# Performance work log

Hardware: AMD Instinct MI355X
Metric: run time of the kernel (lower is better)

The kernel has to match this reference:

```python
import jax, jax.numpy as jnp
import numpy as np

B, T, D = 2, 2048, 1024
HEADS, UNITS = 16, 64
OUT_DIM = 1024
_LARGE_BIAS = 10000.0


def _uniform(key, shape, fan_in, fan_out):
    limit = np.sqrt(6.0 / (fan_in + fan_out))
    return jax.random.uniform(key, shape, jnp.float32, -limit, limit)


def setup_inputs() -> dict:
    key = jax.random.key(0)
    kx, kq, kk, kv, ko = jax.random.split(key, 5)
    x = jax.random.normal(kx, (B, T, D), jnp.float32)
    mask = jnp.ones((B, T), jnp.int32)
    Wq = _uniform(kq, (D, HEADS * UNITS), D, UNITS)
    Wk = _uniform(kk, (D, HEADS * UNITS), D, UNITS)
    Wv = _uniform(kv, (D, HEADS * UNITS), D, UNITS)
    Wo = _uniform(ko, (HEADS * UNITS, OUT_DIM), HEADS * UNITS, OUT_DIM)
    return {"x": x, "mask": mask, "Wq": Wq, "Wk": Wk, "Wv": Wv, "Wo": Wo}


def reference(x, mask, Wq, Wk, Wv, Wo):
    m = mask.astype(x.dtype)                      # [B, T]
    x = x * m[:, :, None]                         # zero padded positions
    b, t, _ = x.shape
    # projections, split heads: [B, T, H, U]
    q = (x @ Wq).reshape(b, t, HEADS, UNITS)
    k = (x @ Wk).reshape(b, t, HEADS, UNITS)
    v = (x @ Wv).reshape(b, t, HEADS, UNITS)
    # logits[b,h,i,j] = sum_u q[b,i,h,u] k[b,j,h,u]
    logits = jnp.einsum('bihu,bjhu->bhij', q, k) / np.sqrt(UNITS).astype(x.dtype)
    # causal (forward) mask: subtract large bias above the diagonal
    causal = jnp.triu(jnp.full((t, t), _LARGE_BIAS, x.dtype), k=1)
    logits = logits - causal
    # padding mask on key axis
    logits = logits - ((1.0 - m) * _LARGE_BIAS)[:, None, None, :]
    weights = jax.nn.softmax(logits, axis=-1)     # [B, H, T, T]
    attended = jnp.einsum('bhij,bjhu->bihu', weights, v)
    attended = attended.reshape(b, t, HEADS * UNITS)
    return attended @ Wo                          # [B, T, OUT_DIM]
```

## Files before the change

kernel.cpp:

```cpp
#include <hip/hip_runtime.h>
#include <stdint.h>
#include <stddef.h>

#define B_ 2
#define T_ 2048
#define D_ 1024
#define H_ 16
#define U_ 64
#define M_ (B_ * T_)
#define N_ (H_ * U_)

typedef __attribute__((ext_vector_type(4))) float f32x4;
typedef __attribute__((ext_vector_type(8))) short s16x8;
typedef __attribute__((ext_vector_type(8))) __bf16 b16x8;

static_assert(sizeof(s16x8) == 16, "frag size");

__device__ __forceinline__ unsigned short f2bf(float f) {
  unsigned int u = __float_as_uint(f);
  u += 0x7FFFu + ((u >> 16) & 1u);
  return (unsigned short)(u >> 16);
}

__device__ __forceinline__ float exp2_hw(float x) {
  float r;
  asm("v_exp_f32 %0, %1" : "=v"(r) : "v"(x));
  return r;
}
__device__ __forceinline__ unsigned int cvtpk_bf16(float lo, float hi) {
  unsigned int r;
  asm("v_cvt_pk_bf16_f32 %0, %1, %2" : "=v"(r) : "v"(lo), "v"(hi));
  return r;
}

template <typename V>
__device__ __forceinline__ auto mfma16_impl(V a, V b, f32x4 c, int)
    -> decltype(__builtin_amdgcn_mfma_f32_16x16x32_bf16(a, b, c, 0, 0, 0)) {
  return __builtin_amdgcn_mfma_f32_16x16x32_bf16(a, b, c, 0, 0, 0);
}
template <typename V>
__device__ __forceinline__ f32x4 mfma16_impl(V a, V b, f32x4 c, long) {
  return __builtin_amdgcn_mfma_f32_16x16x32_bf16(
      __builtin_bit_cast(b16x8, a), __builtin_bit_cast(b16x8, b), c, 0, 0, 0);
}
__device__ __forceinline__ f32x4 mfma16(s16x8 a, s16x8 b, f32x4 c) {
  return mfma16_impl(a, b, c, 0);
}

__device__ __forceinline__ void gld16(const unsigned short* g, unsigned short* l) {
  __builtin_amdgcn_global_load_lds(
      (const __attribute__((address_space(1))) void*)g,
      (__attribute__((address_space(3))) void*)l, 16, 0, 0);
}

__global__ void wtrans_kernel(const float* __restrict__ w0, const float* __restrict__ w1,
                              const float* __restrict__ w2, const float* __restrict__ w3,
                              unsigned short* __restrict__ o0, unsigned short* __restrict__ o1,
                              unsigned short* __restrict__ o2, unsigned short* __restrict__ o3) {
  __shared__ float tile[64][65];
  const float* w;
  unsigned short* o;
  switch (blockIdx.z) {
    case 0: w = w0; o = o0; break;
    case 1: w = w1; o = o1; break;
    case 2: w = w2; o = o2; break;
    default: w = w3; o = o3; break;
  }
  const int kb = blockIdx.y * 64, nb = blockIdx.x * 64;
  const int tid = threadIdx.x;
  const int r0 = tid >> 6, c = tid & 63;
#pragma unroll
  for (int i = 0; i < 16; i++) {
    int r = i * 4 + r0;
    tile[r][c] = w[(size_t)(kb + r) * 1024 + nb + c];
  }
  __syncthreads();
#pragma unroll
  for (int i = 0; i < 16; i++) {
    int r = i * 4 + r0;
    o[(size_t)(nb + r) * 1024 + kb + c] = f2bf(tile[c][r]);
  }
}

__global__ void xmask_kernel(const float* __restrict__ x, const int* __restrict__ mask,
                             unsigned short* __restrict__ xb) {
  const int idx = (blockIdx.x * 256 + threadIdx.x) * 4;
  const int row = idx >> 10;
  const float m = (float)mask[row];
  float4 v = *(const float4*)(x + idx);
  ushort4 o;
  o.x = f2bf(v.x * m);
  o.y = f2bf(v.y * m);
  o.z = f2bf(v.z * m);
  o.w = f2bf(v.w * m);
  *(ushort4*)(xb + idx) = o;
}

template <int MODE>
__device__ __forceinline__ void gemm97_body(const unsigned short* __restrict__ A,
                                            const unsigned short* __restrict__ Bt,
                                            void* __restrict__ Cout) {
  constexpr int Kd = 1024, Nd = 1024;
  __shared__ unsigned short la[128 * 32];
  __shared__ unsigned short lb[128 * 32];
  const int tid = threadIdx.x;
  const int lane = tid & 63;
  const int w = tid >> 6;
  const int mb = blockIdx.y * 128, nb = blockIdx.x * 128;
  const int wm = (w >> 1) * 64, wn = (w & 1) * 64;
  const int lr = lane & 15, lg = lane >> 4;
  const int srow = w * 16 + (lane >> 2);
  const int scol = (lane & 3) * 8;
  const unsigned short* gA = A + (size_t)(mb + srow) * Kd + scol;
  const unsigned short* gB = Bt + (size_t)(nb + srow) * Kd + scol;
  unsigned short* lA = la + srow * 32 + scol;
  unsigned short* lB = lb + srow * 32 + scol;

  f32x4 acc[4][4] = {};

  for (int kt = 0; kt < Kd; kt += 32) {
    gld16(gA + kt, lA);
    gld16(gA + kt + (size_t)64 * Kd, lA + 64 * 32);
    gld16(gB + kt, lB);
    gld16(gB + kt + (size_t)64 * Kd, lB + 64 * 32);
    __syncthreads();
    s16x8 af[4], bfr[4];
#pragma unroll
    for (int i = 0; i < 4; i++)
      af[i] = *(const s16x8*)(la + (wm + i * 16 + lr) * 32 + lg * 8);
#pragma unroll
    for (int j = 0; j < 4; j++)
      bfr[j] = *(const s16x8*)(lb + (wn + j * 16 + lr) * 32 + lg * 8);
#pragma unroll
    for (int i = 0; i < 4; i++)
#pragma unroll
      for (int j = 0; j < 4; j++)
        acc[i][j] = mfma16(af[i], bfr[j], acc[i][j]);
    __syncthreads();
  }

#pragma unroll
  for (int i = 0; i < 4; i++)
#pragma unroll
    for (int j = 0; j < 4; j++) {
      const int col = nb + wn + j * 16 + lr;
      const int rowb = mb + wm + i * 16 + lg * 4;
      if (MODE == 1) {
        float* C = (float*)Cout;
#pragma unroll
        for (int r = 0; r < 4; r++) C[(size_t)(rowb + r) * Nd + col] = acc[i][j][r];
      } else if (MODE == 0) {
        unsigned short* C = (unsigned short*)Cout;
#pragma unroll
        for (int r = 0; r < 4; r++) C[(size_t)(rowb + r) * Nd + col] = f2bf(acc[i][j][r]);
      } else {
        unsigned short* C = (unsigned short*)Cout;
        const size_t vrow = ((size_t)(rowb >> 11) * 16 + (col >> 6)) * 64 + (col & 63);
        ushort4 o;
#pragma unroll
        for (int r = 0; r < 4; r++) ((unsigned short*)&o)[r] = f2bf(acc[i][j][r]);
        *(ushort4*)(C + vrow * T_ + (rowb & 2047)) = o;
      }
    }
}

__global__ __launch_bounds__(256) void gemm_qkv(const unsigned short* __restrict__ A,
                                                const unsigned short* __restrict__ wq,
                                                const unsigned short* __restrict__ wk,
                                                const unsigned short* __restrict__ wv,
                                                unsigned short* __restrict__ cq,
                                                unsigned short* __restrict__ ck,
                                                unsigned short* __restrict__ vt) {
  if (blockIdx.z == 0) {
    gemm97_body<0>(A, wq, cq);
  } else if (blockIdx.z == 1) {
    gemm97_body<0>(A, wk, ck);
  } else {
    gemm97_body<2>(A, wv, vt);
  }
}

__global__ __launch_bounds__(256) void gemm_out(const unsigned short* __restrict__ A,
                                                const unsigned short* __restrict__ woT,
                                                float* __restrict__ C) {
  gemm97_body<1>(A, woT, C);
}

__global__ __launch_bounds__(64) void attn16_kernel(const unsigned short* __restrict__ Q,
                                                    const unsigned short* __restrict__ K,
                                                    const unsigned short* __restrict__ Vt,
                                                    const int* __restrict__ mask,
                                                    unsigned short* __restrict__ att) {
  __shared__ unsigned short pbuf[32 * 64];
  const int lane = threadIdx.x & 63;
  const int li = lane & 15, lg = lane >> 4;
  const int bh = blockIdx.x & 31;
  const int b = bh >> 4, h = bh & 15;
  const int pr = blockIdx.x >> 5;

  const float CS = 0.125f * 1.44269504089f;
  const float PB = 10000.0f * 1.44269504089f;
  const float THR = 8.0f;

  const unsigned short* Kb = K + (size_t)(b * T_) * 1024 + h * 64;
  const unsigned short* Vtb = Vt + (size_t)bh * 64 * T_;
  const int* mk = mask + b * T_;

  const int xr = (li & 3) << 5;
  char* pbb = (char*)pbuf;

  for (int g = 0; g < 2; g++) {
    const int qg = g == 0 ? (63 - pr) : pr;
    const int q0 = qg * 32;

    s16x8 qf[2][2];
#pragma unroll
    for (int f = 0; f < 2; f++) {
      const unsigned short* qrow = Q + ((size_t)(b * T_) + q0 + f * 16 + li) * 1024 + h * 64;
      qf[f][0] = *(const s16x8*)(qrow + lg * 8);
      qf[f][1] = *(const s16x8*)(qrow + 32 + lg * 8);
    }

    const int iq0 = q0 + li, iq1 = q0 + 16 + li;

    float mrun[2] = {-1e30f, -1e30f};
    f32x4 lp[2] = {};
    f32x4 acc[4][2] = {};

    const int ntiles = (q0 + 95) >> 6;

    auto loadK = [&](s16x8 (&dst)[4][2], int jb) {
#pragma unroll
      for (int jf = 0; jf < 4; jf++) {
        const unsigned short* kr = Kb + (size_t)(jb + jf * 16 + li) * 1024 + lg * 8;
        dst[jf][0] = *(const s16x8*)kr;
        dst[jf][1] = *(const s16x8*)(kr + 32);
      }
    };

    s16x8 kA[4][2], kB[4][2];
    loadK(kA, 0);

    auto body = [&](int t, s16x8 (&kc)[4][2], s16x8 (&kn)[4][2]) {
      const int jb = t * 64;
      const bool diag = (jb + 64 > q0);

      int4 mv[4];
#pragma unroll
      for (int jf = 0; jf < 4; jf++)
        mv[jf] = *(const int4*)(mk + jb + jf * 16 + lg * 4);

      f32x4 s[4][2] = {};
      __builtin_amdgcn_s_setprio(1);
#pragma unroll
      for (int jf = 0; jf < 4; jf++) {
        s[jf][0] = mfma16(kc[jf][0], qf[0][0], s[jf][0]);
        s[jf][0] = mfma16(kc[jf][1], qf[0][1], s[jf][0]);
        s[jf][1] = mfma16(kc[jf][0], qf[1][0], s[jf][1]);
        s[jf][1] = mfma16(kc[jf][1], qf[1][1], s[jf][1]);
      }
      __builtin_amdgcn_s_setprio(0);

      if (t + 1 < ntiles) loadK(kn, jb + 64);

      s16x8 vf[4][2];
#pragma unroll
      for (int uf = 0; uf < 4; uf++) {
        const unsigned short* vr = Vtb + (size_t)(uf * 16 + li) * T_ + jb + lg * 8;
        vf[uf][0] = *(const s16x8*)vr;
        vf[uf][1] = *(const s16x8*)(vr + 32);
      }

      const int band = (mv[0].x & mv[0].y & mv[0].z & mv[0].w) &
                       (mv[1].x & mv[1].y & mv[1].z & mv[1].w) &
                       (mv[2].x & mv[2].y & mv[2].z & mv[2].w) &
                       (mv[3].x & mv[3].y & mv[3].z & mv[3].w);
      const bool noBias = __all(band != 0);

#pragma unroll
      for (int f = 0; f < 2; f++) {
        const int iq = f ? iq1 : iq0;
        f32x4 pv = {-3e38f, -3e38f, -3e38f, -3e38f};
        if (noBias) {
#pragma unroll
          for (int jf = 0; jf < 4; jf++) {
            f32x4 zz = s[jf][f] * CS;
            if (diag) {
#pragma unroll
              for (int r = 0; r < 4; r++)
                if (jb + jf * 16 + lg * 4 + r > iq) zz[r] = -1e30f;
            }
            s[jf][f] = zz;
            pv = __builtin_elementwise_max(pv, zz);
          }
        } else {
#pragma unroll
          for (int jf = 0; jf < 4; jf++) {
            f32x4 zz;
#pragma unroll
            for (int r = 0; r < 4; r++) {
              float z = fmaf(s[jf][f][r], CS, ((&mv[jf].x)[r] ? 0.f : -PB));
              if (diag && (jb + jf * 16 + lg * 4 + r > iq)) z = -1e30f;
              zz[r] = z;
            }
            s[jf][f] = zz;
            pv = __builtin_elementwise_max(pv, zz);
          }
        }
        const float pmax = fmaxf(fmaxf(pv[0], pv[1]), fmaxf(pv[2], pv[3]));
        if (!__all(pmax <= mrun[f] + THR)) {
          float rmax = fmaxf(pmax, __shfl_xor(pmax, 16));
          rmax = fmaxf(rmax, __shfl_xor(rmax, 32));
          const float mnew = fmaxf(mrun[f], rmax);
          const float al = exp2_hw(mrun[f] - mnew);
          lp[f] *= al;
#pragma unroll
          for (int uf = 0; uf < 4; uf++) acc[uf][f] *= al;
          mrun[f] = mnew;
        }
        const float mm = mrun[f];
#pragma unroll
        for (int jf = 0; jf < 4; jf++) {
          f32x4 p;
#pragma unroll
          for (int r = 0; r < 4; r++) p[r] = exp2_hw(s[jf][f][r] - mm);
          lp[f] += p;
          uint2 w2;
          w2.x = cvtpk_bf16(p[0], p[1]);
          w2.y = cvtpk_bf16(p[2], p[3]);
          const int wb = (((f * 16 + li) * 64 + jf * 16 + lg * 4) * 2) ^ xr;
          *(uint2*)(pbb + wb) = w2;
        }
      }

      s16x8 pfrag[2][2];
#pragma unroll
      for (int f = 0; f < 2; f++)
#pragma unroll
        for (int hh = 0; hh < 2; hh++) {
          const int rd = (((f * 16 + li) * 64 + hh * 32 + lg * 8) * 2) ^ xr;
          pfrag[f][hh] = *(const s16x8*)(pbb + rd);
        }
      __builtin_amdgcn_s_setprio(1);
#pragma unroll
      for (int uf = 0; uf < 4; uf++)
#pragma unroll
        for (int f = 0; f < 2; f++) {
          acc[uf][f] = mfma16(vf[uf][0], pfrag[f][0], acc[uf][f]);
          acc[uf][f] = mfma16(vf[uf][1], pfrag[f][1], acc[uf][f]);
        }
      __builtin_amdgcn_s_setprio(0);
    };

    int t = 0;
    for (; t + 1 < ntiles; t += 2) {
      body(t, kA, kB);
      body(t + 1, kB, kA);
    }
    if (t < ntiles) body(t, kA, kB);

#pragma unroll
    for (int f = 0; f < 2; f++) {
      float l = (lp[f][0] + lp[f][1]) + (lp[f][2] + lp[f][3]);
      l += __shfl_xor(l, 16);
      l += __shfl_xor(l, 32);
      const float inv = 1.0f / l;
      unsigned short* arow = att + ((size_t)(b * T_) + q0 + f * 16 + li) * 1024 + h * 64;
#pragma unroll
      for (int uf = 0; uf < 4; uf++) {
        ushort4 o;
#pragma unroll
        for (int r = 0; r < 4; r++)
          ((unsigned short*)&o)[r] = __builtin_bit_cast(unsigned short, (__bf16)(acc[uf][f][r] * inv));
        *(ushort4*)(arow + uf * 16 + lg * 4) = o;
      }
    }
  }
}

extern "C" void kernel_launch(void* const* d_in, const int* in_sizes, int n_in,
                              void* d_out, int out_size, void* d_ws, size_t ws_size,
                              hipStream_t stream) {
  const float* x = (const float*)d_in[0];
  const int* mask = (const int*)d_in[1];
  const float* Wq = (const float*)d_in[2];
  const float* Wk = (const float*)d_in[3];
  const float* Wv = (const float*)d_in[4];
  const float* Wo = (const float*)d_in[5];

  const size_t MB = 1u << 20;
  char* ws = (char*)d_ws;
  unsigned short* wqT = (unsigned short*)(ws + 0 * MB);
  unsigned short* wkT = (unsigned short*)(ws + 2 * MB);
  unsigned short* wvT = (unsigned short*)(ws + 4 * MB);
  unsigned short* woT = (unsigned short*)(ws + 6 * MB);
  unsigned short* xb  = (unsigned short*)(ws + 8 * MB);
  unsigned short* qb  = (unsigned short*)(ws + 16 * MB);
  unsigned short* kb  = (unsigned short*)(ws + 24 * MB);
  unsigned short* vt  = (unsigned short*)(ws + 32 * MB);
  unsigned short* att = xb;
  (void)ws_size; (void)in_sizes; (void)n_in; (void)out_size;

  wtrans_kernel<<<dim3(16, 16, 4), 256, 0, stream>>>(Wq, Wk, Wv, Wo, wqT, wkT, wvT, woT);
  xmask_kernel<<<dim3(4096), 256, 0, stream>>>(x, mask, xb);
  gemm_qkv<<<dim3(8, 32, 3), 256, 0, stream>>>(xb, wqT, wkT, wvT, qb, kb, vt);
  attn16_kernel<<<dim3(1024), 64, 0, stream>>>(qb, kb, vt, mask, att);
  gemm_out<<<dim3(8, 32), 256, 0, stream>>>(att, woT, (float*)d_out);
}
```

Baseline: 142.9 us.

## Software-pipeline QK^T MFMA of next tile with softmax of current tile

Restructures the attention inner loop into stages (load K/mask, QK MFMA, softmax, PV MFMA) and issues the QK^T MFMAs for tile t+1 before the PV of tile t, with double-buffered score and mask registers. The aim is to overlap MFMA work with the exp/max VALU work of the softmax, and to prefetch mask and K two tiles ahead. This raises register pressure (two score buffers plus two K buffers), which could spill or lower occupancy in a 64-thread block.

```diff
diff --git a/kernel.cpp b/kernel.cpp
--- a/kernel.cpp
+++ b/kernel.cpp
@@ -186,7 +186,7 @@
   gemm97_body<1>(A, woT, C);
 }
 
-__global__ __launch_bounds__(64) void attn16_kernel(const unsigned short* __restrict__ Q,
+__global__ __launch_bounds__(64) void attn17_kernel(const unsigned short* __restrict__ Q,
                                                     const unsigned short* __restrict__ K,
                                                     const unsigned short* __restrict__ Vt,
                                                     const int* __restrict__ mask,
@@ -226,6 +226,7 @@
     float mrun[2] = {-1e30f, -1e30f};
     f32x4 lp[2] = {};
     f32x4 acc[4][2] = {};
+    s16x8 vf[4][2];
 
     const int ntiles = (q0 + 95) >> 6;
 
@@ -237,50 +238,43 @@
         dst[jf][1] = *(const s16x8*)(kr + 32);
       }
     };
-
-    s16x8 kA[4][2], kB[4][2];
-    loadK(kA, 0);
-
-    auto body = [&](int t, s16x8 (&kc)[4][2], s16x8 (&kn)[4][2]) {
-      const int jb = t * 64;
-      const bool diag = (jb + 64 > q0);
-
-      int4 mv[4];
+    auto loadM = [&](int4 (&dst)[4], int jb) {
 #pragma unroll
       for (int jf = 0; jf < 4; jf++)
-        mv[jf] = *(const int4*)(mk + jb + jf * 16 + lg * 4);
-
-      f32x4 s[4][2] = {};
-      __builtin_amdgcn_s_setprio(1);
-#pragma unroll
-      for (int jf = 0; jf < 4; jf++) {
-        s[jf][0] = mfma16(kc[jf][0], qf[0][0], s[jf][0]);
-        s[jf][0] = mfma16(kc[jf][1], qf[0][1], s[jf][0]);
-        s[jf][1] = mfma16(kc[jf][0], qf[1][0], s[jf][1]);
-        s[jf][1] = mfma16(kc[jf][1], qf[1][1], s[jf][1]);
-      }
-      __builtin_amdgcn_s_setprio(0);
-
-      if (t + 1 < ntiles) loadK(kn, jb + 64);
-
-      s16x8 vf[4][2];
+        dst[jf] = *(const int4*)(mk + jb + jf * 16 + lg * 4);
+    };
+    auto loadV = [&](int jb) {
 #pragma unroll
       for (int uf = 0; uf < 4; uf++) {
         const unsigned short* vr = Vtb + (size_t)(uf * 16 + li) * T_ + jb + lg * 8;
         vf[uf][0] = *(const s16x8*)vr;
         vf[uf][1] = *(const s16x8*)(vr + 32);
       }
-
+    };
+    auto qk = [&](f32x4 (&s)[4][2], s16x8 (&kc)[4][2]) {
+      __builtin_amdgcn_s_setprio(1);
+#pragma unroll
+      for (int jf = 0; jf < 4; jf++) {
+        f32x4 z = {};
+        s[jf][0] = mfma16(kc[jf][0], qf[0][0], z);
+        s[jf][0] = mfma16(kc[jf][1], qf[0][1], s[jf][0]);
+        f32x4 z2 = {};
+        s[jf][1] = mfma16(kc[jf][0], qf[1][0], z2);
+        s[jf][1] = mfma16(kc[jf][1], qf[1][1], s[jf][1]);
+      }
+      __builtin_amdgcn_s_setprio(0);
+    };
+    auto smw = [&](f32x4 (&s)[4][2], int4 (&mv)[4], int jb) {
+      const bool diag = (jb + 64 > q0);
       const int band = (mv[0].x & mv[0].y & mv[0].z & mv[0].w) &
                        (mv[1].x & mv[1].y & mv[1].z & mv[1].w) &
                        (mv[2].x & mv[2].y & mv[2].z & mv[2].w) &
                        (mv[3].x & mv[3].y & mv[3].z & mv[3].w);
       const bool noBias = __all(band != 0);
-
 #pragma unroll
       for (int f = 0; f < 2; f++) {
         const int iq = f ? iq1 : iq0;
-        f32x4 pv = {-3e38f, -3e38f, -3e38f, -3e38f};
+        f32x4 pv4 = {-3e38f, -3e38f, -3e38f, -3e38f};
         if (noBias) {
 #pragma unroll
           for (int jf = 0; jf < 4; jf++) {
@@ -291,7 +285,7 @@
                 if (jb + jf * 16 + lg * 4 + r > iq) zz[r] = -1e30f;
             }
             s[jf][f] = zz;
-            pv = __builtin_elementwise_max(pv, zz);
+            pv4 = __builtin_elementwise_max(pv4, zz);
           }
         } else {
 #pragma unroll
@@ -304,10 +298,10 @@
               zz[r] = z;
             }
             s[jf][f] = zz;
-            pv = __builtin_elementwise_max(pv, zz);
+            pv4 = __builtin_elementwise_max(pv4, zz);
           }
         }
-        const float pmax = fmaxf(fmaxf(pv[0], pv[1]), fmaxf(pv[2], pv[3]));
+        const float pmax = fmaxf(fmaxf(pv4[0], pv4[1]), fmaxf(pv4[2], pv4[3]));
         if (!__all(pmax <= mrun[f] + THR)) {
           float rmax = fmaxf(pmax, __shfl_xor(pmax, 16));
           rmax = fmaxf(rmax, __shfl_xor(rmax, 32));
@@ -332,7 +326,8 @@
           *(uint2*)(pbb + wb) = w2;
         }
       }
-
+    };
+    auto pv = [&]() {
       s16x8 pfrag[2][2];
 #pragma unroll
       for (int f = 0; f < 2; f++)
@@ -352,12 +347,46 @@
       __builtin_amdgcn_s_setprio(0);
     };
 
+    s16x8 kA[4][2], kB[4][2];
+    f32x4 sA[4][2], sB[4][2];
+    int4 mA[4], mB[4];
+
+    loadK(kA, 0);
+    loadM(mA, 0);
+    qk(sA, kA);
+    if (ntiles > 1) {
+      loadK(kB, 64);
+      loadM(mB, 64);
+    }
+
     int t = 0;
-    for (; t + 1 < ntiles; t += 2) {
-      body(t, kA, kB);
-      body(t + 1, kB, kA);
+    while (true) {
+      {
+        const int jb = t * 64;
+        loadV(jb);
+        smw(sA, mA, jb);
+        if (t + 1 < ntiles) qk(sB, kB);
+        if (t + 2 < ntiles) {
+          loadK(kA, (t + 2) * 64);
+          loadM(mA, (t + 2) * 64);
+        }
+        pv();
+      }
+      if (t + 1 >= ntiles) break;
+      {
+        const int jb = (t + 1) * 64;
+        loadV(jb);
+        smw(sB, mB, jb);
+        if (t + 2 < ntiles) qk(sA, kA);
+        if (t + 3 < ntiles) {
+          loadK(kB, (t + 3) * 64);
+          loadM(mB, (t + 3) * 64);
+        }
+        pv();
+      }
+      t += 2;
+      if (t >= ntiles) break;
     }
-    if (t < ntiles) body(t, kA, kB);
 
 #pragma unroll
     for (int f = 0; f < 2; f++) {
@@ -404,6 +433,6 @@
   wtrans_kernel<<<dim3(16, 16, 4), 256, 0, stream>>>(Wq, Wk, Wv, Wo, wqT, wkT, wvT, woT);
   xmask_kernel<<<dim3(4096), 256, 0, stream>>>(x, mask, xb);
   gemm_qkv<<<dim3(8, 32, 3), 256, 0, stream>>>(xb, wqT, wkT, wvT, qb, kb, vt);
-  attn16_kernel<<<dim3(1024), 64, 0, stream>>>(qb, kb, vt, mask, att);
+  attn17_kernel<<<dim3(1024), 64, 0, stream>>>(qb, kb, vt, mask, att);
   gemm_out<<<dim3(8, 32), 256, 0, stream>>>(att, woT, (float*)d_out);
 }
```

Result: no change. 141.1 us (-1.3%).
